# Performance work log

Measured on AMD Instinct MI355X. Metric: run time of the kernel, lower is better.

Reference implementation:

```python
import jax, jax.numpy as jnp
import numpy as np
from jax import lax

B, S, D, F, E, K = 4, 2048, 2048, 8192, 8, 2


def setup_inputs() -> dict:
    key = jax.random.key(0)
    ks = jax.random.split(key, 4)
    sd = 1.0 / np.sqrt(D)
    sf = 1.0 / np.sqrt(F)
    return {
        "hidden_states": jax.random.normal(ks[0], (B, S, D), dtype=jnp.float32),
        "router_w": jax.random.normal(ks[1], (D, E), dtype=jnp.float32) * sd,
        "w1": jax.random.normal(ks[2], (E, D, F), dtype=jnp.float32) * sd,
        "b1": jnp.zeros((E, F), dtype=jnp.float32),
        "w2": jax.random.normal(ks[3], (E, F, D), dtype=jnp.float32) * sf,
        "b2": jnp.zeros((E, D), dtype=jnp.float32),
        "top_k": K,
    }


def reference(hidden_states, router_w, w1, b1, w2, b2, top_k):
    b, s, d = hidden_states.shape
    x = hidden_states.reshape(-1, d)  # [T, D] flat tokens
    # Router: top-k over expert logits, softmax over the selected logits.
    logits = x @ router_w                      # [T, E]
    top_vals, top_idx = lax.top_k(logits, top_k)  # [T, K]
    scores = jax.nn.softmax(top_vals, axis=-1)    # [T, K]

    out = jnp.zeros_like(x)
    n_experts = w1.shape[0]
    for e in range(n_experts):  # fixed small expert count
        # per-token combine weight for this expert (0 if not routed)
        cw = jnp.sum(jnp.where(top_idx == e, scores, 0.0), axis=-1)  # [T]
        h = jax.nn.gelu(x @ w1[e] + b1[e], approximate=False)        # [T, F]
        out = out + cw[:, None] * (h @ w2[e] + b2[e])                # masked combine
    out = out.reshape(b, s, d)
    return out + hidden_states  # use_residual=True
```

## Files before the change

kernel.cpp:

```cpp
#include <hip/hip_runtime.h>

#define T_TOK 8192
#define DIM   2048
#define FFN   8192
#define NE    8
#define TOPK  2

typedef unsigned short ushort_t;
typedef unsigned short ushort8  __attribute__((ext_vector_type(8)));
typedef unsigned short ushort4v __attribute__((ext_vector_type(4)));
typedef short bf16x8 __attribute__((ext_vector_type(8)));
typedef float f32x4  __attribute__((ext_vector_type(4)));

__device__ __forceinline__ ushort_t f2bf(float f) {
  unsigned int u = __float_as_uint(f);
  u += 0x7FFFu + ((u >> 16) & 1u);
  return (ushort_t)(u >> 16);
}
__device__ __forceinline__ float bf2f(ushort_t u) {
  return __uint_as_float(((unsigned int)u) << 16);
}

__device__ __forceinline__ void gload16(const void* g, void* l) {
  __builtin_amdgcn_global_load_lds((const __attribute__((address_space(1))) void*)g,
                                   (__attribute__((address_space(3))) void*)l, 16, 0, 0);
}

__device__ __forceinline__ float gelu_exact(float v) {
  float s = v * 0.70710678118654752f;
  float a = fabsf(s);
  float t = __builtin_amdgcn_rcpf(1.0f + 0.3275911f * a);
  float p = t * (0.254829592f +
            t * (-0.284496736f +
            t * (1.421413741f +
            t * (-1.453152027f +
            t * 1.061405429f))));
  float er = 1.0f - p * __expf(-a * a);
  er = copysignf(er, s);
  return 0.5f * v * (1.0f + er);
}

__global__ __launch_bounds__(256) void k_router(
    const float* __restrict__ x, const float* __restrict__ rw, ushort_t* __restrict__ xbf,
    int* __restrict__ tidx, float* __restrict__ twt, int* __restrict__ counts) {
  int t = blockIdx.x;
  int tid = threadIdx.x;
  int lane = tid & 63, wave = tid >> 6;
  float acc[NE];
#pragma unroll
  for (int e = 0; e < NE; e++) acc[e] = 0.f;
  const float* xr = x + (size_t)t * DIM;
  ushort_t* xbr = xbf + (size_t)t * DIM;
#pragma unroll
  for (int it = 0; it < 2; it++) {
    int d4 = it * 1024 + tid * 4;
    float4 v = *reinterpret_cast<const float4*>(xr + d4);
    ushort4v o;
    o.x = f2bf(v.x); o.y = f2bf(v.y); o.z = f2bf(v.z); o.w = f2bf(v.w);
    *reinterpret_cast<ushort4v*>(xbr + d4) = o;
    const float* r0p = rw + (size_t)d4 * NE;
    float xv[4] = {v.x, v.y, v.z, v.w};
#pragma unroll
    for (int j = 0; j < 4; j++) {
      const float* r = r0p + j * NE;
#pragma unroll
      for (int e = 0; e < NE; e++) acc[e] += xv[j] * r[e];
    }
  }
  __shared__ float wsum[4][NE];
#pragma unroll
  for (int e = 0; e < NE; e++) {
    float v = acc[e];
#pragma unroll
    for (int off = 32; off > 0; off >>= 1) v += __shfl_down(v, off);
    if (lane == 0) wsum[wave][e] = v;
  }
  __syncthreads();
  if (tid == 0) {
    float lg[NE];
#pragma unroll
    for (int e = 0; e < NE; e++) lg[e] = wsum[0][e] + wsum[1][e] + wsum[2][e] + wsum[3][e];
    int i0 = 0; float v0 = lg[0];
#pragma unroll
    for (int e = 1; e < NE; e++) if (lg[e] > v0) { v0 = lg[e]; i0 = e; }
    int i1 = -1; float v1 = -3.4e38f;
#pragma unroll
    for (int e = 0; e < NE; e++) if (e != i0 && lg[e] > v1) { v1 = lg[e]; i1 = e; }
    float e1 = expf(v1 - v0);
    float s = 1.f + e1;
    tidx[t * 2 + 0] = i0; tidx[t * 2 + 1] = i1;
    twt[t * 2 + 0] = 1.f / s; twt[t * 2 + 1] = e1 / s;
    atomicAdd(&counts[i0], 1);
    atomicAdd(&counts[i1], 1);
  }
}

#define TT 64
__global__ __launch_bounds__(256) void k_wcvt(const float* __restrict__ in,
                                              ushort_t* __restrict__ outp, int R, int C) {
  __shared__ float t[TT][TT + 1];
  int e = blockIdx.z;
  const float* src = in + (size_t)e * R * C;
  ushort_t* dst = outp + (size_t)e * R * C;
  int r0 = blockIdx.y * TT, c0 = blockIdx.x * TT;
  int tid = threadIdx.x;
  int rr = tid >> 4;
  int c4 = tid & 15;
#pragma unroll
  for (int i = 0; i < 4; i++) {
    int r = rr + i * 16;
    float4 v = *reinterpret_cast<const float4*>(src + (size_t)(r0 + r) * C + c0 + c4 * 4);
    t[r][c4 * 4 + 0] = v.x; t[r][c4 * 4 + 1] = v.y;
    t[r][c4 * 4 + 2] = v.z; t[r][c4 * 4 + 3] = v.w;
  }
  __syncthreads();
  int c = tid >> 2, rs = tid & 3;
  ushort8 v0, v1;
#pragma unroll
  for (int i = 0; i < 8; i++) {
    v0[i] = f2bf(t[rs * 16 + i][c]);
    v1[i] = f2bf(t[rs * 16 + 8 + i][c]);
  }
  ushort_t* drow = dst + (size_t)(c0 + c) * R + r0 + rs * 16;
  *reinterpret_cast<ushort8*>(drow) = v0;
  *reinterpret_cast<ushort8*>(drow + 8) = v1;
}

__global__ void k_scan(const int* __restrict__ counts, int* __restrict__ offsets) {
  if (threadIdx.x == 0) {
    int s = 0;
    for (int e = 0; e < NE; e++) { offsets[e] = s; s += counts[e]; }
    offsets[NE] = s;
  }
}

__global__ void k_fill(const int* __restrict__ tidx, const float* __restrict__ twt,
                       const int* __restrict__ offsets, int* __restrict__ cursors,
                       int* __restrict__ ltok, float* __restrict__ lwt, int* __restrict__ ppos) {
  int t = blockIdx.x * blockDim.x + threadIdx.x;
  if (t >= T_TOK) return;
#pragma unroll
  for (int k = 0; k < TOPK; k++) {
    int e = tidx[t * 2 + k];
    int pos = atomicAdd(&cursors[e], 1);
    int p = offsets[e] + pos;
    ltok[p] = t;
    lwt[p] = twt[t * 2 + k];
    ppos[t * 2 + k] = p;
  }
}

#define BM 128
#define BN 128
#define BK 32

__device__ __forceinline__ void xcd_decode(int lin, int nwg, int nx, int& xt, int& yt) {
  int q = nwg >> 3;
  int w = (lin & 7) * q + (lin >> 3);
  xt = w % nx;
  yt = w / nx;
}

__global__ __launch_bounds__(256) void k_gemm1(
    const ushort_t* __restrict__ xbf, const ushort_t* __restrict__ w1t, const float* __restrict__ b1,
    const int* __restrict__ counts, const int* __restrict__ offsets,
    const int* __restrict__ ltok, ushort_t* __restrict__ H) {
  int e = blockIdx.z;
  int cnt = counts[e];
  int xt, yt;
  xcd_decode(blockIdx.x, (T_TOK / BM) * (FFN / BN), T_TOK / BM, xt, yt);
  int row0 = xt * BM;
  if (row0 >= cnt) return;
  int base = offsets[e];
  int col0 = yt * BN;
  const ushort_t* Bt = w1t + (size_t)e * DIM * FFN;

  __shared__ __align__(16) ushort_t As[BM * BK];
  __shared__ __align__(16) ushort_t Bs[BM * BK];

  int tid = threadIdx.x;
  int wave = tid >> 6, lane = tid & 63;
  int wm = wave >> 1, wn = wave & 1;
  int lm = lane & 15, lg = lane >> 4;

  int srow = tid >> 2, seg = tid & 3;
  const ushort_t* asrc[2]; const ushort_t* bsrc[2];
#pragma unroll
  for (int j = 0; j < 2; j++) {
    int ar = min(row0 + j * 64 + srow, cnt - 1);
    asrc[j] = xbf + (size_t)ltok[base + ar] * DIM + seg * 8;
    bsrc[j] = Bt + (size_t)(col0 + j * 64 + srow) * DIM + seg * 8;
  }
  f32x4 acc[4][4];
#pragma unroll
  for (int m = 0; m < 4; m++)
#pragma unroll
    for (int n = 0; n < 4; n++) acc[m][n] = (f32x4){0.f, 0.f, 0.f, 0.f};

  for (int k0 = 0; k0 < DIM; k0 += BK) {
#pragma unroll
    for (int j = 0; j < 2; j++) {
      gload16(asrc[j] + k0, &As[(j * 256 + wave * 64) * 8]);
      gload16(bsrc[j] + k0, &Bs[(j * 256 + wave * 64) * 8]);
    }
    __syncthreads();
    bf16x8 af[4], bfv[4];
#pragma unroll
    for (int m = 0; m < 4; m++)
      af[m] = *reinterpret_cast<const bf16x8*>(&As[(wm * 64 + m * 16 + lm) * BK + lg * 8]);
#pragma unroll
    for (int n = 0; n < 4; n++)
      bfv[n] = *reinterpret_cast<const bf16x8*>(&Bs[(wn * 64 + n * 16 + lm) * BK + lg * 8]);
#pragma unroll
    for (int m = 0; m < 4; m++)
#pragma unroll
      for (int n = 0; n < 4; n++)
        acc[m][n] = __builtin_amdgcn_mfma_f32_16x16x32_bf16(af[m], bfv[n], acc[m][n], 0, 0, 0);
    __syncthreads();
  }
#pragma unroll
  for (int m = 0; m < 4; m++) {
#pragma unroll
    for (int n = 0; n < 4; n++) {
      int f = col0 + wn * 64 + n * 16 + lm;
      float bias = b1[e * FFN + f];
#pragma unroll
      for (int r = 0; r < 4; r++) {
        int row = row0 + wm * 64 + m * 16 + lg * 4 + r;
        if (row < cnt) {
          float v = acc[m][n][r] + bias;
          H[(size_t)(base + row) * FFN + f] = f2bf(gelu_exact(v));
        }
      }
    }
  }
}

__global__ __launch_bounds__(256) void k_gemm2(
    const ushort_t* __restrict__ H, const ushort_t* __restrict__ w2t, const float* __restrict__ b2,
    const int* __restrict__ counts, const int* __restrict__ offsets,
    const float* __restrict__ lwt, ushort_t* __restrict__ contrib) {
  int e = blockIdx.z;
  int cnt = counts[e];
  int xt, yt;
  xcd_decode(blockIdx.x, (T_TOK / BM) * (DIM / BN), T_TOK / BM, xt, yt);
  int row0 = xt * BM;
  if (row0 >= cnt) return;
  int base = offsets[e];
  int col0 = yt * BN;
  const ushort_t* Bt = w2t + (size_t)e * DIM * FFN;

  __shared__ __align__(16) ushort_t As[BM * BK];
  __shared__ __align__(16) ushort_t Bs[BM * BK];

  int tid = threadIdx.x;
  int wave = tid >> 6, lane = tid & 63;
  int wm = wave >> 1, wn = wave & 1;
  int lm = lane & 15, lg = lane >> 4;

  int srow = tid >> 2, seg = tid & 3;
  const ushort_t* asrc[2]; const ushort_t* bsrc[2];
#pragma unroll
  for (int j = 0; j < 2; j++) {
    int ar = min(row0 + j * 64 + srow, cnt - 1);
    asrc[j] = H + (size_t)(base + ar) * FFN + seg * 8;
    bsrc[j] = Bt + (size_t)(col0 + j * 64 + srow) * FFN + seg * 8;
  }
  f32x4 acc[4][4];
#pragma unroll
  for (int m = 0; m < 4; m++)
#pragma unroll
    for (int n = 0; n < 4; n++) acc[m][n] = (f32x4){0.f, 0.f, 0.f, 0.f};

  for (int k0 = 0; k0 < FFN; k0 += BK) {
#pragma unroll
    for (int j = 0; j < 2; j++) {
      gload16(asrc[j] + k0, &As[(j * 256 + wave * 64) * 8]);
      gload16(bsrc[j] + k0, &Bs[(j * 256 + wave * 64) * 8]);
    }
    __syncthreads();
    bf16x8 af[4], bfv[4];
#pragma unroll
    for (int m = 0; m < 4; m++)
      af[m] = *reinterpret_cast<const bf16x8*>(&As[(wm * 64 + m * 16 + lm) * BK + lg * 8]);
#pragma unroll
    for (int n = 0; n < 4; n++)
      bfv[n] = *reinterpret_cast<const bf16x8*>(&Bs[(wn * 64 + n * 16 + lm) * BK + lg * 8]);
#pragma unroll
    for (int m = 0; m < 4; m++)
#pragma unroll
      for (int n = 0; n < 4; n++)
        acc[m][n] = __builtin_amdgcn_mfma_f32_16x16x32_bf16(af[m], bfv[n], acc[m][n], 0, 0, 0);
    __syncthreads();
  }
#pragma unroll
  for (int m = 0; m < 4; m++) {
#pragma unroll
    for (int n = 0; n < 4; n++) {
      int d = col0 + wn * 64 + n * 16 + lm;
      float bias = b2[e * DIM + d];
#pragma unroll
      for (int r = 0; r < 4; r++) {
        int row = row0 + wm * 64 + m * 16 + lg * 4 + r;
        if (row < cnt) {
          float v = (acc[m][n][r] + bias) * lwt[base + row];
          contrib[(size_t)(base + row) * DIM + d] = f2bf(v);
        }
      }
    }
  }
}

__global__ void k_combine(const float* __restrict__ x, const ushort_t* __restrict__ contrib,
                          const int* __restrict__ ppos, float* __restrict__ out) {
  int i = blockIdx.x * blockDim.x + threadIdx.x;
  int t = i / (DIM / 4);
  int dq = i % (DIM / 4);
  int p0 = ppos[t * 2 + 0], p1 = ppos[t * 2 + 1];
  float4 xv = reinterpret_cast<const float4*>(x)[i];
  ushort4v c0 = reinterpret_cast<const ushort4v*>(contrib + (size_t)p0 * DIM)[dq];
  ushort4v c1 = reinterpret_cast<const ushort4v*>(contrib + (size_t)p1 * DIM)[dq];
  float4 o;
  o.x = xv.x + bf2f(c0.x) + bf2f(c1.x);
  o.y = xv.y + bf2f(c0.y) + bf2f(c1.y);
  o.z = xv.z + bf2f(c0.z) + bf2f(c1.z);
  o.w = xv.w + bf2f(c0.w) + bf2f(c1.w);
  reinterpret_cast<float4*>(out)[i] = o;
}

extern "C" void kernel_launch(void* const* d_in, const int* in_sizes, int n_in,
                              void* d_out, int out_size, void* d_ws, size_t ws_size,
                              hipStream_t stream) {
  const float* x  = (const float*)d_in[0];
  const float* rw = (const float*)d_in[1];
  const float* w1 = (const float*)d_in[2];
  const float* b1 = (const float*)d_in[3];
  const float* w2 = (const float*)d_in[4];
  const float* b2 = (const float*)d_in[5];
  float* out = (float*)d_out;
  char* ws = (char*)d_ws;

  const size_t MB = 1u << 20;
  int*   counts  = (int*)(ws);
  int*   offsets = (int*)(ws + 64);
  int*   cursors = (int*)(ws + 128);
  int*   tidx    = (int*)(ws + 1 * MB);
  float* twt     = (float*)(ws + 2 * MB);
  int*   ltok    = (int*)(ws + 3 * MB);
  float* lwt     = (float*)(ws + 4 * MB);
  int*   ppos    = (int*)(ws + 5 * MB);
  ushort_t* xbf     = (ushort_t*)(ws + 8 * MB);
  ushort_t* contrib = (ushort_t*)(ws + 8 * MB);
  ushort_t* Hbuf    = (ushort_t*)(ws + 72 * MB);
  ushort_t* w1t     = (ushort_t*)(ws + 328 * MB);
  ushort_t* w2t     = (ushort_t*)(ws + 328 * MB);
  const size_t NEED = 584 * MB;
  if (ws_size < NEED) {
    hipMemsetAsync(d_out, 0, (size_t)out_size * sizeof(float), stream);
    return;
  }

  hipMemsetAsync(ws, 0, 256, stream);
  k_router<<<T_TOK, 256, 0, stream>>>(x, rw, xbf, tidx, twt, counts);
  k_scan<<<1, 64, 0, stream>>>(counts, offsets);
  k_fill<<<T_TOK / 256, 256, 0, stream>>>(tidx, twt, offsets, cursors, ltok, lwt, ppos);
  k_wcvt<<<dim3(FFN / TT, DIM / TT, NE), 256, 0, stream>>>(w1, w1t, DIM, FFN);
  k_gemm1<<<dim3((T_TOK / BM) * (FFN / BN), 1, NE), 256, 0, stream>>>(xbf, w1t, b1, counts, offsets, ltok, Hbuf);
  k_wcvt<<<dim3(DIM / TT, FFN / TT, NE), 256, 0, stream>>>(w2, w2t, FFN, DIM);
  k_gemm2<<<dim3((T_TOK / BM) * (DIM / BN), 1, NE), 256, 0, stream>>>(Hbuf, w2t, b2, counts, offsets, lwt, contrib);
  k_combine<<<dim3((T_TOK * (size_t)DIM / 4) / 256), 256, 0, stream>>>(x, contrib, ppos, out);
}
```

Measured before the change: 2.168 ms.

## Rewrite expert down-projection GEMM as 256x256 pipelined tile with swizzled LDS

Replaces the second expert GEMM's 128x128x32 single-buffered tile with a 256x256x64 tile run by 512 threads (8 waves). It double-buffers A and B in shared memory with asynchronous global-to-LDS loads issued ahead, XOR-swizzles the LDS layout to avoid bank conflicts, and uses inline ds_read_b128, explicit waitcnt and barriers, and setprio around the MFMA blocks. The goal is to hide memory latency and raise data reuse per tile. The cost is more LDS and register pressure (32 accumulators per wave), lower occupancy, and coarser tiles that waste more work on partial expert rows.

Result: faster. 2.121 ms (-2.2%).

```diff
diff --git a/kernel.cpp b/kernel.cpp
--- a/kernel.cpp
+++ b/kernel.cpp
@@ -24,6 +24,14 @@
 __device__ __forceinline__ void gload16(const void* g, void* l) {
   __builtin_amdgcn_global_load_lds((const __attribute__((address_space(1))) void*)g,
                                    (__attribute__((address_space(3))) void*)l, 16, 0, 0);
+}
+__device__ __forceinline__ unsigned lds_off(const ushort_t* p) {
+  return (unsigned)(uintptr_t)(__attribute__((address_space(3))) const ushort_t*)p;
+}
+__device__ __forceinline__ bf16x8 ds_read128(unsigned off) {
+  bf16x8 r;
+  asm volatile("ds_read_b128 %0, %1" : "=v"(r) : "v"(off));
+  return r;
 }
 
 __device__ __forceinline__ float gelu_exact(float v) {
@@ -150,16 +158,16 @@
   }
 }
 
-#define BM 128
-#define BN 128
-#define BK 32
-
 __device__ __forceinline__ void xcd_decode(int lin, int nwg, int nx, int& xt, int& yt) {
   int q = nwg >> 3;
   int w = (lin & 7) * q + (lin >> 3);
   xt = w % nx;
   yt = w / nx;
 }
+
+#define BM 128
+#define BN 128
+#define BK 32
 
 __global__ __launch_bounds__(256) void k_gemm1(
     const ushort_t* __restrict__ xbf, const ushort_t* __restrict__ w1t, const float* __restrict__ b1,
@@ -236,72 +244,144 @@
   }
 }
 
-__global__ __launch_bounds__(256) void k_gemm2(
+#define QBM 256
+#define QBN 256
+#define QBK 64
+#define QHALF_E (128 * 64)
+#define QSLOT_E (2 * QHALF_E)
+
+__global__ __launch_bounds__(512) void k_gemm2(
     const ushort_t* __restrict__ H, const ushort_t* __restrict__ w2t, const float* __restrict__ b2,
     const int* __restrict__ counts, const int* __restrict__ offsets,
     const float* __restrict__ lwt, ushort_t* __restrict__ contrib) {
   int e = blockIdx.z;
   int cnt = counts[e];
   int xt, yt;
-  xcd_decode(blockIdx.x, (T_TOK / BM) * (DIM / BN), T_TOK / BM, xt, yt);
-  int row0 = xt * BM;
+  xcd_decode(blockIdx.x, (T_TOK / QBM) * (DIM / QBN), T_TOK / QBM, xt, yt);
+  int row0 = xt * QBM;
   if (row0 >= cnt) return;
   int base = offsets[e];
-  int col0 = yt * BN;
+  int col0 = yt * QBN;
   const ushort_t* Bt = w2t + (size_t)e * DIM * FFN;
 
-  __shared__ __align__(16) ushort_t As[BM * BK];
-  __shared__ __align__(16) ushort_t Bs[BM * BK];
+  __shared__ __align__(16) ushort_t As[2 * QSLOT_E];
+  __shared__ __align__(16) ushort_t Bs[2 * QSLOT_E];
 
   int tid = threadIdx.x;
-  int wave = tid >> 6, lane = tid & 63;
-  int wm = wave >> 1, wn = wave & 1;
+  int wid = tid >> 6, lane = tid & 63;
+  int wm = wid >> 2, wn = wid & 3;
   int lm = lane & 15, lg = lane >> 4;
 
-  int srow = tid >> 2, seg = tid & 3;
-  const ushort_t* asrc[2]; const ushort_t* bsrc[2];
-#pragma unroll
-  for (int j = 0; j < 2; j++) {
-    int ar = min(row0 + j * 64 + srow, cnt - 1);
-    asrc[j] = H + (size_t)(base + ar) * FFN + seg * 8;
-    bsrc[j] = Bt + (size_t)(col0 + j * 64 + srow) * FFN + seg * 8;
-  }
-  f32x4 acc[4][4];
-#pragma unroll
-  for (int m = 0; m < 4; m++)
+  const ushort_t* aS[2][2]; const ushort_t* bS[2][2];
+#pragma unroll
+  for (int l = 0; l < 2; l++) {
+    int c = l * 512 + tid;
+    int rr = c >> 3;
+    int s8 = (c & 7) ^ (rr & 7);
+#pragma unroll
+    for (int h = 0; h < 2; h++) {
+      int ar = min(row0 + h * 128 + rr, cnt - 1);
+      aS[h][l] = H + (size_t)(base + ar) * FFN + s8 * 8;
+      bS[h][l] = Bt + (size_t)(col0 + h * 128 + rr) * FFN + s8 * 8;
+    }
+  }
+  auto STA = [&](int slot, int h, int k0) {
+#pragma unroll
+    for (int l = 0; l < 2; l++)
+      gload16(aS[h][l] + k0, As + slot * QSLOT_E + h * QHALF_E + (l * 512 + wid * 64) * 8);
+  };
+  auto STB = [&](int slot, int h, int k0) {
+#pragma unroll
+    for (int l = 0; l < 2; l++)
+      gload16(bS[h][l] + k0, Bs + slot * QSLOT_E + h * QHALF_E + (l * 512 + wid * 64) * 8);
+  };
+
+  unsigned abase = lds_off(As), bbase = lds_off(Bs);
+  unsigned aoff[8][2], boff[4][2];
+#pragma unroll
+  for (int m = 0; m < 8; m++)
+#pragma unroll
+    for (int kk = 0; kk < 2; kk++)
+      aoff[m][kk] = abase + (unsigned)((wm * QHALF_E + (m * 16 + lm) * 64 +
+                                        (((kk * 4 + lg) ^ (lm & 7)) * 8)) * 2);
+#pragma unroll
+  for (int n = 0; n < 4; n++)
+#pragma unroll
+    for (int kk = 0; kk < 2; kk++)
+      boff[n][kk] = bbase + (unsigned)(((wn >> 1) * QHALF_E + ((wn & 1) * 64 + n * 16 + lm) * 64 +
+                                        (((kk * 4 + lg) ^ (lm & 7)) * 8)) * 2);
+
+  f32x4 acc[8][4];
+#pragma unroll
+  for (int m = 0; m < 8; m++)
 #pragma unroll
     for (int n = 0; n < 4; n++) acc[m][n] = (f32x4){0.f, 0.f, 0.f, 0.f};
 
-  for (int k0 = 0; k0 < FFN; k0 += BK) {
-#pragma unroll
-    for (int j = 0; j < 2; j++) {
-      gload16(asrc[j] + k0, &As[(j * 256 + wave * 64) * 8]);
-      gload16(bsrc[j] + k0, &Bs[(j * 256 + wave * 64) * 8]);
-    }
-    __syncthreads();
-    bf16x8 af[4], bfv[4];
-#pragma unroll
-    for (int m = 0; m < 4; m++)
-      af[m] = *reinterpret_cast<const bf16x8*>(&As[(wm * 64 + m * 16 + lm) * BK + lg * 8]);
-#pragma unroll
-    for (int n = 0; n < 4; n++)
-      bfv[n] = *reinterpret_cast<const bf16x8*>(&Bs[(wn * 64 + n * 16 + lm) * BK + lg * 8]);
-#pragma unroll
-    for (int m = 0; m < 4; m++)
-#pragma unroll
-      for (int n = 0; n < 4; n++)
-        acc[m][n] = __builtin_amdgcn_mfma_f32_16x16x32_bf16(af[m], bfv[n], acc[m][n], 0, 0, 0);
-    __syncthreads();
-  }
-#pragma unroll
-  for (int m = 0; m < 4; m++) {
+  const int NT = FFN / QBK;
+  STA(0, 0, 0); STA(0, 1, 0);
+  STB(0, 0, 0); STB(0, 1, 0);
+  STB(1, 0, QBK); STB(1, 1, QBK);
+  asm volatile("s_waitcnt vmcnt(4)" ::: "memory");
+  __builtin_amdgcn_s_barrier();
+
+  for (int T = 0; T < NT; ++T) {
+    int slot = T & 1;
+    unsigned cb = (unsigned)(slot * QSLOT_E * 2);
+    bf16x8 bv[4][2];
+#pragma unroll
+    for (int q = 0; q < 4; q++) {
+      bf16x8 af[2][2];
+      if (q == 0) {
+#pragma unroll
+        for (int n = 0; n < 4; n++)
+#pragma unroll
+          for (int kk = 0; kk < 2; kk++) bv[n][kk] = ds_read128(boff[n][kk] + cb);
+      }
+#pragma unroll
+      for (int mf = 0; mf < 2; mf++)
+#pragma unroll
+        for (int kk = 0; kk < 2; kk++)
+          af[mf][kk] = ds_read128(aoff[q * 2 + mf][kk] + cb);
+      if (q == 0 && T + 1 < NT) STA(slot ^ 1, 0, (T + 1) * QBK);
+      if (q == 1) {
+        if (T + 1 < NT) STA(slot ^ 1, 1, (T + 1) * QBK);
+        if (T + 2 < NT) STB(slot, 0, (T + 2) * QBK);
+      }
+      if (q == 2 && T + 2 < NT) STB(slot, 1, (T + 2) * QBK);
+      __builtin_amdgcn_sched_barrier(0);
+      __builtin_amdgcn_s_barrier();
+      asm volatile("s_waitcnt lgkmcnt(0)" ::: "memory");
+      __builtin_amdgcn_sched_barrier(0);
+      __builtin_amdgcn_s_setprio(1);
+#pragma unroll
+      for (int mf = 0; mf < 2; mf++)
+#pragma unroll
+        for (int nf = 0; nf < 4; nf++)
+#pragma unroll
+          for (int kk = 0; kk < 2; kk++)
+            acc[q * 2 + mf][nf] = __builtin_amdgcn_mfma_f32_16x16x32_bf16(
+                af[mf][kk], bv[nf][kk], acc[q * 2 + mf][nf], 0, 0, 0);
+      __builtin_amdgcn_s_setprio(0);
+      __builtin_amdgcn_sched_barrier(0);
+      if (q == 3) {
+        if (T < NT - 2) { asm volatile("s_waitcnt vmcnt(4)" ::: "memory"); }
+        else            { asm volatile("s_waitcnt vmcnt(0)" ::: "memory"); }
+        __builtin_amdgcn_sched_barrier(0);
+      }
+      __builtin_amdgcn_s_barrier();
+      __builtin_amdgcn_sched_barrier(0);
+    }
+  }
+
+#pragma unroll
+  for (int m = 0; m < 8; m++) {
 #pragma unroll
     for (int n = 0; n < 4; n++) {
       int d = col0 + wn * 64 + n * 16 + lm;
       float bias = b2[e * DIM + d];
 #pragma unroll
       for (int r = 0; r < 4; r++) {
-        int row = row0 + wm * 64 + m * 16 + lg * 4 + r;
+        int row = row0 + wm * 128 + m * 16 + lg * 4 + r;
         if (row < cnt) {
           float v = (acc[m][n][r] + bias) * lwt[base + row];
           contrib[(size_t)(base + row) * DIM + d] = f2bf(v);
@@ -367,6 +447,6 @@
   k_wcvt<<<dim3(FFN / TT, DIM / TT, NE), 256, 0, stream>>>(w1, w1t, DIM, FFN);
   k_gemm1<<<dim3((T_TOK / BM) * (FFN / BN), 1, NE), 256, 0, stream>>>(xbf, w1t, b1, counts, offsets, ltok, Hbuf);
   k_wcvt<<<dim3(DIM / TT, FFN / TT, NE), 256, 0, stream>>>(w2, w2t, FFN, DIM);
-  k_gemm2<<<dim3((T_TOK / BM) * (DIM / BN), 1, NE), 256, 0, stream>>>(Hbuf, w2t, b2, counts, offsets, lwt, contrib);
+  k_gemm2<<<dim3((T_TOK / QBM) * (DIM / QBN), 1, NE), 512, 0, stream>>>(Hbuf, w2t, b2, counts, offsets, lwt, contrib);
   k_combine<<<dim3((T_TOK * (size_t)DIM / 4) / 256), 256, 0, stream>>>(x, contrib, ppos, out);
 }
```

## Rewrite expert GEMMs as 256x256 double-buffered, swizzled 8-wave pipelined kernels

Applied to the files above, without the earlier changes.

Both expert GEMMs move from 128x128x32 tiles with 4 waves and a single LDS buffer to 256x256x64 tiles with 8 waves, double-buffered LDS, and XOR-swizzled layouts that avoid bank conflicts. Global-to-LDS loads for the next k-steps are interleaved with MFMA phases, using explicit waitcnt, barriers, setprio and sched_barrier. The aim is to hide memory latency and raise arithmetic intensity per byte loaded. In exchange, register and LDS pressure rise (128KB LDS per block). Larger tiles also waste more work on the partial tile at the end of each expert's token range.

Result: faster. 2.000 ms (-7.8%).

```diff
diff --git a/kernel.cpp b/kernel.cpp
--- a/kernel.cpp
+++ b/kernel.cpp
@@ -24,6 +24,14 @@
 __device__ __forceinline__ void gload16(const void* g, void* l) {
   __builtin_amdgcn_global_load_lds((const __attribute__((address_space(1))) void*)g,
                                    (__attribute__((address_space(3))) void*)l, 16, 0, 0);
+}
+__device__ __forceinline__ unsigned lds_off(const ushort_t* p) {
+  return (unsigned)(uintptr_t)(__attribute__((address_space(3))) const ushort_t*)p;
+}
+__device__ __forceinline__ bf16x8 ds_read128(unsigned off) {
+  bf16x8 r;
+  asm volatile("ds_read_b128 %0, %1" : "=v"(r) : "v"(off));
+  return r;
 }
 
 __device__ __forceinline__ float gelu_exact(float v) {
@@ -150,10 +158,6 @@
   }
 }
 
-#define BM 128
-#define BN 128
-#define BK 32
-
 __device__ __forceinline__ void xcd_decode(int lin, int nwg, int nx, int& xt, int& yt) {
   int q = nwg >> 3;
   int w = (lin & 7) * q + (lin >> 3);
@@ -161,72 +165,150 @@
   yt = w / nx;
 }
 
-__global__ __launch_bounds__(256) void k_gemm1(
+#define QBM 256
+#define QBN 256
+#define QBK 64
+#define QHALF_E (128 * 64)
+#define QSLOT_E (2 * QHALF_E)
+
+#define GEMM8_PIPE(NT_)                                                                 \
+  const int NT = (NT_);                                                                 \
+  STA(0, 0, 0); STA(0, 1, 0);                                                           \
+  STB(0, 0, 0); STB(0, 1, 0);                                                           \
+  STB(1, 0, QBK); STB(1, 1, QBK);                                                       \
+  asm volatile("s_waitcnt vmcnt(4)" ::: "memory");                                      \
+  __builtin_amdgcn_s_barrier();                                                         \
+  for (int T = 0; T < NT; ++T) {                                                        \
+    int slot = T & 1;                                                                   \
+    unsigned cb = (unsigned)(slot * QSLOT_E * 2);                                       \
+    bf16x8 bv[4][2];                                                                    \
+    _Pragma("unroll")                                                                   \
+    for (int q = 0; q < 4; q++) {                                                       \
+      bf16x8 af[2][2];                                                                  \
+      if (q == 0) {                                                                     \
+        _Pragma("unroll")                                                               \
+        for (int n = 0; n < 4; n++) {                                                   \
+          bv[n][0] = ds_read128(boff[n][0] + cb);                                       \
+          bv[n][1] = ds_read128(boff[n][1] + cb);                                       \
+        }                                                                               \
+      }                                                                                 \
+      _Pragma("unroll")                                                                 \
+      for (int mf = 0; mf < 2; mf++) {                                                  \
+        af[mf][0] = ds_read128(aoff[q * 2 + mf][0] + cb);                               \
+        af[mf][1] = ds_read128(aoff[q * 2 + mf][1] + cb);                               \
+      }                                                                                 \
+      if (q == 0 && T + 1 < NT) STA(slot ^ 1, 0, (T + 1) * QBK);                        \
+      if (q == 1) {                                                                     \
+        if (T + 1 < NT) STA(slot ^ 1, 1, (T + 1) * QBK);                                \
+        if (T + 2 < NT) STB(slot, 0, (T + 2) * QBK);                                    \
+      }                                                                                 \
+      if (q == 2 && T + 2 < NT) STB(slot, 1, (T + 2) * QBK);                            \
+      __builtin_amdgcn_sched_barrier(0);                                                \
+      __builtin_amdgcn_s_barrier();                                                     \
+      asm volatile("s_waitcnt lgkmcnt(0)" ::: "memory");                                \
+      __builtin_amdgcn_sched_barrier(0);                                                \
+      __builtin_amdgcn_s_setprio(1);                                                    \
+      _Pragma("unroll")                                                                 \
+      for (int mf = 0; mf < 2; mf++)                                                    \
+        _Pragma("unroll")                                                               \
+        for (int nf = 0; nf < 4; nf++) {                                                \
+          acc[q * 2 + mf][nf] = __builtin_amdgcn_mfma_f32_16x16x32_bf16(                \
+              af[mf][0], bv[nf][0], acc[q * 2 + mf][nf], 0, 0, 0);                      \
+          acc[q * 2 + mf][nf] = __builtin_amdgcn_mfma_f32_16x16x32_bf16(                \
+              af[mf][1], bv[nf][1], acc[q * 2 + mf][nf], 0, 0, 0);                      \
+        }                                                                               \
+      __builtin_amdgcn_s_setprio(0);                                                    \
+      __builtin_amdgcn_sched_barrier(0);                                                \
+      if (q == 3) {                                                                     \
+        if (T < NT - 2) { asm volatile("s_waitcnt vmcnt(4)" ::: "memory"); }            \
+        else            { asm volatile("s_waitcnt vmcnt(0)" ::: "memory"); }            \
+        __builtin_amdgcn_sched_barrier(0);                                              \
+      }                                                                                 \
+      __builtin_amdgcn_s_barrier();                                                     \
+      __builtin_amdgcn_sched_barrier(0);                                                \
+    }                                                                                   \
+  }
+
+#define GEMM8_SETUP()                                                                   \
+  int tid = threadIdx.x;                                                                \
+  int wid = tid >> 6, lane = tid & 63;                                                  \
+  int wm = wid >> 2, wn = wid & 3;                                                      \
+  int lm = lane & 15, lg = lane >> 4;                                                   \
+  unsigned abase = lds_off(As), bbase = lds_off(Bs);                                    \
+  unsigned aoff[8][2], boff[4][2];                                                      \
+  _Pragma("unroll")                                                                     \
+  for (int m = 0; m < 8; m++)                                                           \
+    _Pragma("unroll")                                                                   \
+    for (int kk = 0; kk < 2; kk++)                                                      \
+      aoff[m][kk] = abase + (unsigned)((wm * QHALF_E + (m * 16 + lm) * 64 +             \
+                                        (((kk * 4 + lg) ^ (lm & 7)) * 8)) * 2);         \
+  _Pragma("unroll")                                                                     \
+  for (int n = 0; n < 4; n++)                                                           \
+    _Pragma("unroll")                                                                   \
+    for (int kk = 0; kk < 2; kk++)                                                      \
+      boff[n][kk] = bbase + (unsigned)(((wn >> 1) * QHALF_E +                           \
+                                        ((wn & 1) * 64 + n * 16 + lm) * 64 +            \
+                                        (((kk * 4 + lg) ^ (lm & 7)) * 8)) * 2);         \
+  f32x4 acc[8][4];                                                                      \
+  _Pragma("unroll")                                                                     \
+  for (int m = 0; m < 8; m++)                                                           \
+    _Pragma("unroll")                                                                   \
+    for (int n = 0; n < 4; n++) acc[m][n] = (f32x4){0.f, 0.f, 0.f, 0.f};
+
+__global__ __launch_bounds__(512) void k_gemm1(
     const ushort_t* __restrict__ xbf, const ushort_t* __restrict__ w1t, const float* __restrict__ b1,
     const int* __restrict__ counts, const int* __restrict__ offsets,
     const int* __restrict__ ltok, ushort_t* __restrict__ H) {
   int e = blockIdx.z;
   int cnt = counts[e];
   int xt, yt;
-  xcd_decode(blockIdx.x, (T_TOK / BM) * (FFN / BN), T_TOK / BM, xt, yt);
-  int row0 = xt * BM;
+  xcd_decode(blockIdx.x, (T_TOK / QBM) * (FFN / QBN), T_TOK / QBM, xt, yt);
+  int row0 = xt * QBM;
   if (row0 >= cnt) return;
   int base = offsets[e];
-  int col0 = yt * BN;
+  int col0 = yt * QBN;
   const ushort_t* Bt = w1t + (size_t)e * DIM * FFN;
 
-  __shared__ __align__(16) ushort_t As[BM * BK];
-  __shared__ __align__(16) ushort_t Bs[BM * BK];
-
-  int tid = threadIdx.x;
-  int wave = tid >> 6, lane = tid & 63;
-  int wm = wave >> 1, wn = wave & 1;
-  int lm = lane & 15, lg = lane >> 4;
-
-  int srow = tid >> 2, seg = tid & 3;
-  const ushort_t* asrc[2]; const ushort_t* bsrc[2];
-#pragma unroll
-  for (int j = 0; j < 2; j++) {
-    int ar = min(row0 + j * 64 + srow, cnt - 1);
-    asrc[j] = xbf + (size_t)ltok[base + ar] * DIM + seg * 8;
-    bsrc[j] = Bt + (size_t)(col0 + j * 64 + srow) * DIM + seg * 8;
-  }
-  f32x4 acc[4][4];
-#pragma unroll
-  for (int m = 0; m < 4; m++)
-#pragma unroll
-    for (int n = 0; n < 4; n++) acc[m][n] = (f32x4){0.f, 0.f, 0.f, 0.f};
-
-  for (int k0 = 0; k0 < DIM; k0 += BK) {
-#pragma unroll
-    for (int j = 0; j < 2; j++) {
-      gload16(asrc[j] + k0, &As[(j * 256 + wave * 64) * 8]);
-      gload16(bsrc[j] + k0, &Bs[(j * 256 + wave * 64) * 8]);
+  __shared__ __align__(16) ushort_t As[2 * QSLOT_E];
+  __shared__ __align__(16) ushort_t Bs[2 * QSLOT_E];
+
+  const ushort_t* aS[2][2]; const ushort_t* bS[2][2];
+#pragma unroll
+  for (int l = 0; l < 2; l++) {
+    int c = l * 512 + threadIdx.x;
+    int rr = c >> 3;
+    int s8 = (c & 7) ^ (rr & 7);
+#pragma unroll
+    for (int h = 0; h < 2; h++) {
+      int ar = min(row0 + h * 128 + rr, cnt - 1);
+      aS[h][l] = xbf + (size_t)ltok[base + ar] * DIM + s8 * 8;
+      bS[h][l] = Bt + (size_t)(col0 + h * 128 + rr) * DIM + s8 * 8;
     }
-    __syncthreads();
-    bf16x8 af[4], bfv[4];
-#pragma unroll
-    for (int m = 0; m < 4; m++)
-      af[m] = *reinterpret_cast<const bf16x8*>(&As[(wm * 64 + m * 16 + lm) * BK + lg * 8]);
-#pragma unroll
-    for (int n = 0; n < 4; n++)
-      bfv[n] = *reinterpret_cast<const bf16x8*>(&Bs[(wn * 64 + n * 16 + lm) * BK + lg * 8]);
-#pragma unroll
-    for (int m = 0; m < 4; m++)
-#pragma unroll
-      for (int n = 0; n < 4; n++)
-        acc[m][n] = __builtin_amdgcn_mfma_f32_16x16x32_bf16(af[m], bfv[n], acc[m][n], 0, 0, 0);
-    __syncthreads();
-  }
-#pragma unroll
-  for (int m = 0; m < 4; m++) {
+  }
+  int swid = threadIdx.x >> 6;
+  auto STA = [&](int slot, int h, int k0) {
+#pragma unroll
+    for (int l = 0; l < 2; l++)
+      gload16(aS[h][l] + k0, As + slot * QSLOT_E + h * QHALF_E + (l * 512 + swid * 64) * 8);
+  };
+  auto STB = [&](int slot, int h, int k0) {
+#pragma unroll
+    for (int l = 0; l < 2; l++)
+      gload16(bS[h][l] + k0, Bs + slot * QSLOT_E + h * QHALF_E + (l * 512 + swid * 64) * 8);
+  };
+
+  GEMM8_SETUP();
+  GEMM8_PIPE(DIM / QBK);
+
+#pragma unroll
+  for (int m = 0; m < 8; m++) {
 #pragma unroll
     for (int n = 0; n < 4; n++) {
       int f = col0 + wn * 64 + n * 16 + lm;
       float bias = b1[e * FFN + f];
 #pragma unroll
       for (int r = 0; r < 4; r++) {
-        int row = row0 + wm * 64 + m * 16 + lg * 4 + r;
+        int row = row0 + wm * 128 + m * 16 + lg * 4 + r;
         if (row < cnt) {
           float v = acc[m][n][r] + bias;
           H[(size_t)(base + row) * FFN + f] = f2bf(gelu_exact(v));
@@ -236,72 +318,60 @@
   }
 }
 
-__global__ __launch_bounds__(256) void k_gemm2(
+__global__ __launch_bounds__(512) void k_gemm2(
     const ushort_t* __restrict__ H, const ushort_t* __restrict__ w2t, const float* __restrict__ b2,
     const int* __restrict__ counts, const int* __restrict__ offsets,
     const float* __restrict__ lwt, ushort_t* __restrict__ contrib) {
   int e = blockIdx.z;
   int cnt = counts[e];
   int xt, yt;
-  xcd_decode(blockIdx.x, (T_TOK / BM) * (DIM / BN), T_TOK / BM, xt, yt);
-  int row0 = xt * BM;
+  xcd_decode(blockIdx.x, (T_TOK / QBM) * (DIM / QBN), T_TOK / QBM, xt, yt);
+  int row0 = xt * QBM;
   if (row0 >= cnt) return;
   int base = offsets[e];
-  int col0 = yt * BN;
+  int col0 = yt * QBN;
   const ushort_t* Bt = w2t + (size_t)e * DIM * FFN;
 
-  __shared__ __align__(16) ushort_t As[BM * BK];
-  __shared__ __align__(16) ushort_t Bs[BM * BK];
-
-  int tid = threadIdx.x;
-  int wave = tid >> 6, lane = tid & 63;
-  int wm = wave >> 1, wn = wave & 1;
-  int lm = lane & 15, lg = lane >> 4;
-
-  int srow = tid >> 2, seg = tid & 3;
-  const ushort_t* asrc[2]; const ushort_t* bsrc[2];
-#pragma unroll
-  for (int j = 0; j < 2; j++) {
-    int ar = min(row0 + j * 64 + srow, cnt - 1);
-    asrc[j] = H + (size_t)(base + ar) * FFN + seg * 8;
-    bsrc[j] = Bt + (size_t)(col0 + j * 64 + srow) * FFN + seg * 8;
-  }
-  f32x4 acc[4][4];
-#pragma unroll
-  for (int m = 0; m < 4; m++)
-#pragma unroll
-    for (int n = 0; n < 4; n++) acc[m][n] = (f32x4){0.f, 0.f, 0.f, 0.f};
-
-  for (int k0 = 0; k0 < FFN; k0 += BK) {
-#pragma unroll
-    for (int j = 0; j < 2; j++) {
-      gload16(asrc[j] + k0, &As[(j * 256 + wave * 64) * 8]);
-      gload16(bsrc[j] + k0, &Bs[(j * 256 + wave * 64) * 8]);
+  __shared__ __align__(16) ushort_t As[2 * QSLOT_E];
+  __shared__ __align__(16) ushort_t Bs[2 * QSLOT_E];
+
+  const ushort_t* aS[2][2]; const ushort_t* bS[2][2];
+#pragma unroll
+  for (int l = 0; l < 2; l++) {
+    int c = l * 512 + threadIdx.x;
+    int rr = c >> 3;
+    int s8 = (c & 7) ^ (rr & 7);
+#pragma unroll
+    for (int h = 0; h < 2; h++) {
+      int ar = min(row0 + h * 128 + rr, cnt - 1);
+      aS[h][l] = H + (size_t)(base + ar) * FFN + s8 * 8;
+      bS[h][l] = Bt + (size_t)(col0 + h * 128 + rr) * FFN + s8 * 8;
     }
-    __syncthreads();
-    bf16x8 af[4], bfv[4];
-#pragma unroll
-    for (int m = 0; m < 4; m++)
-      af[m] = *reinterpret_cast<const bf16x8*>(&As[(wm * 64 + m * 16 + lm) * BK + lg * 8]);
-#pragma unroll
-    for (int n = 0; n < 4; n++)
-      bfv[n] = *reinterpret_cast<const bf16x8*>(&Bs[(wn * 64 + n * 16 + lm) * BK + lg * 8]);
-#pragma unroll
-    for (int m = 0; m < 4; m++)
-#pragma unroll
-      for (int n = 0; n < 4; n++)
-        acc[m][n] = __builtin_amdgcn_mfma_f32_16x16x32_bf16(af[m], bfv[n], acc[m][n], 0, 0, 0);
-    __syncthreads();
-  }
-#pragma unroll
-  for (int m = 0; m < 4; m++) {
+  }
+  int swid = threadIdx.x >> 6;
+  auto STA = [&](int slot, int h, int k0) {
+#pragma unroll
+    for (int l = 0; l < 2; l++)
+      gload16(aS[h][l] + k0, As + slot * QSLOT_E + h * QHALF_E + (l * 512 + swid * 64) * 8);
+  };
+  auto STB = [&](int slot, int h, int k0) {
+#pragma unroll
+    for (int l = 0; l < 2; l++)
+      gload16(bS[h][l] + k0, Bs + slot * QSLOT_E + h * QHALF_E + (l * 512 + swid * 64) * 8);
+  };
+
+  GEMM8_SETUP();
+  GEMM8_PIPE(FFN / QBK);
+
+#pragma unroll
+  for (int m = 0; m < 8; m++) {
 #pragma unroll
     for (int n = 0; n < 4; n++) {
       int d = col0 + wn * 64 + n * 16 + lm;
       float bias = b2[e * DIM + d];
 #pragma unroll
       for (int r = 0; r < 4; r++) {
-        int row = row0 + wm * 64 + m * 16 + lg * 4 + r;
+        int row = row0 + wm * 128 + m * 16 + lg * 4 + r;
         if (row < cnt) {
           float v = (acc[m][n][r] + bias) * lwt[base + row];
           contrib[(size_t)(base + row) * DIM + d] = f2bf(v);
@@ -365,8 +435,8 @@
   k_scan<<<1, 64, 0, stream>>>(counts, offsets);
   k_fill<<<T_TOK / 256, 256, 0, stream>>>(tidx, twt, offsets, cursors, ltok, lwt, ppos);
   k_wcvt<<<dim3(FFN / TT, DIM / TT, NE), 256, 0, stream>>>(w1, w1t, DIM, FFN);
-  k_gemm1<<<dim3((T_TOK / BM) * (FFN / BN), 1, NE), 256, 0, stream>>>(xbf, w1t, b1, counts, offsets, ltok, Hbuf);
+  k_gemm1<<<dim3((T_TOK / QBM) * (FFN / QBN), 1, NE), 512, 0, stream>>>(xbf, w1t, b1, counts, offsets, ltok, Hbuf);
   k_wcvt<<<dim3(DIM / TT, FFN / TT, NE), 256, 0, stream>>>(w2, w2t, FFN, DIM);
-  k_gemm2<<<dim3((T_TOK / BM) * (DIM / BN), 1, NE), 256, 0, stream>>>(Hbuf, w2t, b2, counts, offsets, lwt, contrib);
+  k_gemm2<<<dim3((T_TOK / QBM) * (DIM / QBN), 1, NE), 512, 0, stream>>>(Hbuf, w2t, b2, counts, offsets, lwt, contrib);
   k_combine<<<dim3((T_TOK * (size_t)DIM / 4) / 256), 256, 0, stream>>>(x, contrib, ppos, out);
 }
```
